# Optimization experiments

Hardware: AMD Instinct MI355X
Metric: run time of the kernel (lower is better)

The kernel has to match this reference:

```python
import jax, jax.numpy as jnp
import numpy as np

N = 50000   # total nodes across batch of graphs
E = 600000  # edges (avg degree 12)
D = 128     # feature dim
L = 3       # GNN layers
B = 64      # number of graphs


def setup_inputs() -> dict:
    key = jax.random.key(0)
    ks = jax.random.split(key, 9)
    x = jax.random.normal(ks[0], (N, D), dtype=jnp.float32)
    edge_index = jax.random.randint(ks[1], (2, E), 0, N)
    batch = jnp.sort(jax.random.randint(ks[2], (N,), 0, B))
    # hard one-hot architecture gates (output of ST gumbel-softmax)
    z_agg = jax.nn.one_hot(jax.random.randint(ks[3], (L,), 0, 3), 3, dtype=jnp.float32)
    z_pool = jax.nn.one_hot(jax.random.randint(ks[4], (), 0, 3), 3, dtype=jnp.float32)
    scale = 1.0 / np.sqrt(D)
    W1 = jax.random.normal(ks[5], (L, D, D), dtype=jnp.float32) * scale
    b1 = jnp.zeros((L, D), dtype=jnp.float32)
    W2 = jax.random.normal(ks[6], (L, D, D), dtype=jnp.float32) * scale
    b2 = jnp.zeros((L, D), dtype=jnp.float32)
    return {"x": x, "edge_index": edge_index, "batch": batch,
            "z_agg": z_agg, "z_pool": z_pool,
            "W1": W1, "b1": b1, "W2": W2, "b2": b2}


def reference(x, edge_index, batch, z_agg, z_pool, W1, b1, W2, b2):
    src, dst = edge_index[0], edge_index[1]
    ones_e = jnp.ones((E,), dtype=x.dtype)
    deg = jax.ops.segment_sum(ones_e, dst, num_segments=N)          # [N]
    deg_c = jnp.maximum(deg, 1.0)[:, None]
    has_nb = (deg > 0)[:, None]

    for l in range(L):
        msg = x[src]                                                # [E, D] gather
        s = jax.ops.segment_sum(msg, dst, num_segments=N)           # sum aggr
        m = s / deg_c                                               # mean aggr
        mx = jax.ops.segment_max(msg, dst, num_segments=N)          # max aggr
        mx = jnp.where(has_nb, mx, 0.0)                             # PyG fills empty with 0
        agg = z_agg[l, 0] * s + z_agg[l, 1] * m + z_agg[l, 2] * mx
        # combine='sum' then FeedForwardNetwork: Linear->relu->Linear
        h = x + agg
        h = jnp.maximum(h @ W1[l] + b1[l], 0.0)
        h = h @ W2[l] + b2[l]
        # act='relu', layer_connect='skip_sum'
        x = x + jnp.maximum(h, 0.0)

    # global pooling mixture over batch vector
    ps = jax.ops.segment_sum(x, batch, num_segments=B)              # [B, D]
    cnt = jax.ops.segment_sum(jnp.ones((N,), x.dtype), batch, num_segments=B)
    pm = ps / jnp.maximum(cnt, 1.0)[:, None]
    pmx = jax.ops.segment_max(x, batch, num_segments=B)
    pmx = jnp.where((cnt > 0)[:, None], pmx, 0.0)
    return z_pool[0] * ps + z_pool[1] * pm + z_pool[2] * pmx
```

## Files before the change

kernel.cpp:

```cpp
#include <hip/hip_runtime.h>
#include <cfloat>

#define DD 128
#define NLAYERS 3
#define NPB 128
#define SCHUNK 1024

typedef short bf16x8 __attribute__((ext_vector_type(8)));
typedef float f32x4 __attribute__((ext_vector_type(4)));

__device__ __forceinline__ unsigned short f2b(float f) {
    unsigned u = __float_as_uint(f);
    u += 0x7fffu + ((u >> 16) & 1u);
    return (unsigned short)(u >> 16);
}
__device__ __forceinline__ float b2f(unsigned short b) {
    return __uint_as_float(((unsigned)b) << 16);
}

__device__ __forceinline__ unsigned enc_f(float f) {
    unsigned b = __float_as_uint(f);
    return (b & 0x80000000u) ? ~b : (b | 0x80000000u);
}
__device__ __forceinline__ float dec_f(unsigned u) {
    return __uint_as_float((u & 0x80000000u) ? (u & 0x7fffffffu) : ~u);
}

__global__ void convert_xb_kernel(const float* __restrict__ in,
                                  unsigned short* __restrict__ xb,
                                  int* __restrict__ deg,
                                  float* __restrict__ ps, unsigned* __restrict__ pmx,
                                  int* __restrict__ cnt,
                                  int n4, int nN, int nBD, int nB) {
    int i = blockIdx.x * blockDim.x + threadIdx.x;
    if (i < n4) {
        float4 v = ((const float4*)in)[i];
        ushort4 b;
        b.x = f2b(v.x); b.y = f2b(v.y); b.z = f2b(v.z); b.w = f2b(v.w);
        ((ushort4*)xb)[i] = b;
    }
    if (i < nN) deg[i] = 0;
    if (i < nBD) { ps[i] = 0.f; pmx[i] = 0u; }
    if (i < nB) cnt[i] = 0;
}

__global__ void convert_w_kernel(const float* __restrict__ W1s, const float* __restrict__ W2s,
                                 unsigned short* __restrict__ Wb1s,
                                 unsigned short* __restrict__ Wb2s, int per) {
    int idx = blockIdx.x * blockDim.x + threadIdx.x;
    if (idx >= 2 * per) return;
    const float* W = (idx < per) ? W1s : W2s;
    unsigned short* Wb = (idx < per) ? Wb1s : Wb2s;
    if (idx >= per) idx -= per;
    int lane = idx & 63;
    int rest = idx >> 6;
    int ks = rest & 3; rest >>= 2;
    int nt = rest & 7;
    int l  = rest >> 3;
    int n = nt * 16 + (lane & 15);
    int kbase = ks * 32 + (lane >> 4) * 8;
    const float* Wl = W + (size_t)l * DD * DD;
    unsigned short* dst = Wb + (size_t)l * DD * DD + ((size_t)(nt * 4 + ks) * 64 + lane) * 8;
#pragma unroll
    for (int j = 0; j < 8; ++j) dst[j] = f2b(Wl[(size_t)(kbase + j) * DD + n]);
}


__global__ void deg_kernel(const int* __restrict__ dst, int* __restrict__ deg, int nE) {
    int e = blockIdx.x * blockDim.x + threadIdx.x;
    if (e < nE) atomicAdd(&deg[dst[e]], 1);
}

__global__ __launch_bounds__(256) void scan_sum_kernel(const int* __restrict__ deg,
                                                       int* __restrict__ bsum, int nN) {
    int t = threadIdx.x;
    int base = blockIdx.x * SCHUNK + t * 4;
    int v = 0;
#pragma unroll
    for (int k = 0; k < 4; ++k) { int i = base + k; if (i < nN) v += deg[i]; }
    for (int off = 32; off; off >>= 1) v += __shfl_down(v, off, 64);
    __shared__ int wsum[4];
    if ((t & 63) == 0) wsum[t >> 6] = v;
    __syncthreads();
    if (t == 0) bsum[blockIdx.x] = wsum[0] + wsum[1] + wsum[2] + wsum[3];
}

__global__ __launch_bounds__(256) void scan_top_kernel(const int* __restrict__ bsum,
                                                       int* __restrict__ boff,
                                                       int* __restrict__ row_ptr,
                                                       int G, int nN) {
    __shared__ int sh[256];
    int t = threadIdx.x;
    int v = (t < G) ? bsum[t] : 0;
    sh[t] = v;
    __syncthreads();
    for (int off = 1; off < 256; off <<= 1) {
        int o = (t >= off) ? sh[t - off] : 0;
        __syncthreads();
        sh[t] += o;
        __syncthreads();
    }
    if (t < G) boff[t] = sh[t] - v;
    if (t == 255) row_ptr[nN] = sh[255];
}

__global__ __launch_bounds__(256) void scan_apply_kernel(const int* __restrict__ deg,
                                                         const int* __restrict__ boff,
                                                         int* __restrict__ row_ptr, int nN) {
    __shared__ int sh[256];
    int t = threadIdx.x;
    int base = blockIdx.x * SCHUNK + t * 4;
    int d0 = 0, d1 = 0, d2 = 0, d3 = 0;
    if (base + 0 < nN) d0 = deg[base + 0];
    if (base + 1 < nN) d1 = deg[base + 1];
    if (base + 2 < nN) d2 = deg[base + 2];
    if (base + 3 < nN) d3 = deg[base + 3];
    int tsum = d0 + d1 + d2 + d3;
    sh[t] = tsum;
    __syncthreads();
    for (int off = 1; off < 256; off <<= 1) {
        int o = (t >= off) ? sh[t - off] : 0;
        __syncthreads();
        sh[t] += o;
        __syncthreads();
    }
    int run = boff[blockIdx.x] + sh[t] - tsum;
    if (base + 0 < nN) row_ptr[base + 0] = run;           run += d0;
    if (base + 1 < nN) row_ptr[base + 1] = run;           run += d1;
    if (base + 2 < nN) row_ptr[base + 2] = run;           run += d2;
    if (base + 3 < nN) row_ptr[base + 3] = run;
}

__global__ void fill_kernel(const int* __restrict__ src, const int* __restrict__ dst,
                            const int* __restrict__ row_ptr, int* __restrict__ deg,
                            int* __restrict__ csr_src, int nE) {
    int e = blockIdx.x * blockDim.x + threadIdx.x;
    if (e >= nE) return;
    int d = dst[e];
    int pos = row_ptr[d] + atomicSub(&deg[d], 1) - 1;
    csr_src[pos] = src[e];
}

__global__ __launch_bounds__(256) void agg_combine_kernel(const unsigned short* __restrict__ xb,
                                                          const int* __restrict__ csr_src,
                                                          const int* __restrict__ row_ptr,
                                                          const float* __restrict__ z_agg_l,
                                                          unsigned short* __restrict__ h0b,
                                                          int nN) {
    int t = threadIdx.x;
    int n = blockIdx.x * 8 + (t >> 5);
    if (n >= nN) return;
    int q = t & 31;
    int start = row_ptr[n], end = row_ptr[n + 1];
    float za0 = z_agg_l[0], za1 = z_agg_l[1], za2 = z_agg_l[2];

    const ushort4* tab = (const ushort4*)xb;
    float4 sum = make_float4(0.f, 0.f, 0.f, 0.f);
    float4 mx  = make_float4(-FLT_MAX, -FLT_MAX, -FLT_MAX, -FLT_MAX);
    int last = end - 1;
    for (int e = start; e < end; e += 8) {
        int s0 = csr_src[e];
        int s1 = csr_src[e + 1 <= last ? e + 1 : last];
        int s2 = csr_src[e + 2 <= last ? e + 2 : last];
        int s3 = csr_src[e + 3 <= last ? e + 3 : last];
        int s4 = csr_src[e + 4 <= last ? e + 4 : last];
        int s5 = csr_src[e + 5 <= last ? e + 5 : last];
        int s6 = csr_src[e + 6 <= last ? e + 6 : last];
        int s7 = csr_src[e + 7 <= last ? e + 7 : last];
        ushort4 v0 = tab[(size_t)s0 * 32 + q];
        ushort4 v1 = tab[(size_t)s1 * 32 + q];
        ushort4 v2 = tab[(size_t)s2 * 32 + q];
        ushort4 v3 = tab[(size_t)s3 * 32 + q];
        ushort4 v4 = tab[(size_t)s4 * 32 + q];
        ushort4 v5 = tab[(size_t)s5 * 32 + q];
        ushort4 v6 = tab[(size_t)s6 * 32 + q];
        ushort4 v7 = tab[(size_t)s7 * 32 + q];
#define ACCP(vb, ok) { float ax=b2f(vb.x),ay=b2f(vb.y),az=b2f(vb.z),aw=b2f(vb.w); \
                  mx.x=fmaxf(mx.x,ax);mx.y=fmaxf(mx.y,ay); \
                  mx.z=fmaxf(mx.z,az);mx.w=fmaxf(mx.w,aw); \
                  if (ok) { sum.x+=ax;sum.y+=ay;sum.z+=az;sum.w+=aw; } }
        ACCP(v0, true)
        ACCP(v1, e + 1 < end)
        ACCP(v2, e + 2 < end)
        ACCP(v3, e + 3 < end)
        ACCP(v4, e + 4 < end)
        ACCP(v5, e + 5 < end)
        ACCP(v6, e + 6 < end)
        ACCP(v7, e + 7 < end)
#undef ACCP
    }
    int degn = end - start;
    float inv = 1.0f / fmaxf((float)degn, 1.0f);
    float c01 = za0 + za1 * inv;
    bool nb = (degn > 0);
    ushort4 sb = tab[(size_t)n * 32 + q];
    ushort4 r;
    r.x = f2b(b2f(sb.x) + c01 * sum.x + za2 * (nb ? mx.x : 0.f));
    r.y = f2b(b2f(sb.y) + c01 * sum.y + za2 * (nb ? mx.y : 0.f));
    r.z = f2b(b2f(sb.z) + c01 * sum.z + za2 * (nb ? mx.z : 0.f));
    r.w = f2b(b2f(sb.w) + c01 * sum.w + za2 * (nb ? mx.w : 0.f));
    ((ushort4*)(h0b + (size_t)n * DD))[q] = r;
}

__global__ __launch_bounds__(256) void fused_ffn_kernel(
        const unsigned short* __restrict__ h0b,
        const unsigned short* __restrict__ Wb1, const float* __restrict__ b1,
        const unsigned short* __restrict__ Wb2, const float* __restrict__ b2,
        const unsigned short* __restrict__ xb_in,
        unsigned short* __restrict__ xb_out, int M) {
    __shared__ char lds[64 * DD * 4];

    int t = threadIdx.x;
    int lane = t & 63;
    int w = t >> 6;
    int row0 = blockIdx.x * 64;
    int ar = row0 + w * 16 + (lane & 15);
    if (ar > M - 1) ar = M - 1;
    int g = lane >> 4;
    int colw = lane & 15;
    int rbl = w * 16 + g * 4;

    const unsigned short* Ap = h0b + (size_t)ar * DD + g * 8;
    bf16x8 a0 = *(const bf16x8*)(Ap);
    bf16x8 a1 = *(const bf16x8*)(Ap + 32);
    bf16x8 a2 = *(const bf16x8*)(Ap + 64);
    bf16x8 a3 = *(const bf16x8*)(Ap + 96);

    const bf16x8* Wv1 = (const bf16x8*)Wb1;
#pragma unroll
    for (int nt = 0; nt < 8; ++nt) {
        f32x4 acc = {0.f, 0.f, 0.f, 0.f};
        acc = __builtin_amdgcn_mfma_f32_16x16x32_bf16(a0, Wv1[(nt * 4 + 0) * 64 + lane], acc, 0, 0, 0);
        acc = __builtin_amdgcn_mfma_f32_16x16x32_bf16(a1, Wv1[(nt * 4 + 1) * 64 + lane], acc, 0, 0, 0);
        acc = __builtin_amdgcn_mfma_f32_16x16x32_bf16(a2, Wv1[(nt * 4 + 2) * 64 + lane], acc, 0, 0, 0);
        acc = __builtin_amdgcn_mfma_f32_16x16x32_bf16(a3, Wv1[(nt * 4 + 3) * 64 + lane], acc, 0, 0, 0);
        float bv = b1[nt * 16 + colw];
        int cb = (nt * 16 + colw) * 2;
#pragma unroll
        for (int i = 0; i < 4; ++i) {
            int r1 = rbl + i;
            *(unsigned short*)(lds + r1 * 256 + (cb ^ ((unsigned)(r1 & 7) << 4))) =
                f2b(fmaxf(acc[i] + bv, 0.f));
        }
    }

    int rAl = w * 16 + (lane & 15);
    unsigned swA = (unsigned)(rAl & 7) << 4;
    const char* hA = lds + rAl * 256;
    bf16x8 c0 = *(const bf16x8*)(hA + ((g * 16 +   0) ^ swA));
    bf16x8 c1 = *(const bf16x8*)(hA + ((g * 16 +  64) ^ swA));
    bf16x8 c2 = *(const bf16x8*)(hA + ((g * 16 + 128) ^ swA));
    bf16x8 c3 = *(const bf16x8*)(hA + ((g * 16 + 192) ^ swA));
    __syncthreads();

    const bf16x8* Wv2 = (const bf16x8*)Wb2;
#pragma unroll
    for (int nt = 0; nt < 8; ++nt) {
        f32x4 acc = {0.f, 0.f, 0.f, 0.f};
        acc = __builtin_amdgcn_mfma_f32_16x16x32_bf16(c0, Wv2[(nt * 4 + 0) * 64 + lane], acc, 0, 0, 0);
        acc = __builtin_amdgcn_mfma_f32_16x16x32_bf16(c1, Wv2[(nt * 4 + 1) * 64 + lane], acc, 0, 0, 0);
        acc = __builtin_amdgcn_mfma_f32_16x16x32_bf16(c2, Wv2[(nt * 4 + 2) * 64 + lane], acc, 0, 0, 0);
        acc = __builtin_amdgcn_mfma_f32_16x16x32_bf16(c3, Wv2[(nt * 4 + 3) * 64 + lane], acc, 0, 0, 0);
        float bv = b2[nt * 16 + colw];
        int cb = (nt * 16 + colw) * 4;
#pragma unroll
        for (int i = 0; i < 4; ++i) {
            int r1 = rbl + i;
            *(float*)(lds + r1 * 512 + (cb ^ ((unsigned)(r1 & 7) << 4))) =
                fmaxf(acc[i] + bv, 0.f);
        }
    }
    __syncthreads();

    int q = t & 31;
    int grp = t >> 5;
    for (int pass = 0; pass < 8; ++pass) {
        int rr = pass * 8 + grp;
        int n = row0 + rr;
        if (n < M) {
            ushort4 xv = ((const ushort4*)(xb_in + (size_t)n * DD))[q];
            float4 vv = *(const float4*)(lds + rr * 512 + ((q * 16) ^ ((unsigned)(rr & 7) << 4)));
            ushort4 b;
            b.x = f2b(b2f(xv.x) + vv.x);
            b.y = f2b(b2f(xv.y) + vv.y);
            b.z = f2b(b2f(xv.z) + vv.z);
            b.w = f2b(b2f(xv.w) + vv.w);
            ((ushort4*)(xb_out + (size_t)n * DD))[q] = b;
        }
    }
}

__global__ __launch_bounds__(256) void pool_partial_kernel(const unsigned short* __restrict__ xb,
                                                           const int* __restrict__ batch,
                                                           float* __restrict__ ps,
                                                           unsigned* __restrict__ pmx,
                                                           int* __restrict__ cnt, int nN) {
    int t = threadIdx.x;
    int q = t & 31;
    int p = t >> 5;
    int node0 = blockIdx.x * NPB;
    int nodeEnd = node0 + NPB; if (nodeEnd > nN) nodeEnd = nN;

    const ushort4* xv = (const ushort4*)xb;
    float4 sum = make_float4(0.f, 0.f, 0.f, 0.f);
    float4 mx  = make_float4(-FLT_MAX, -FLT_MAX, -FLT_MAX, -FLT_MAX);
    int count = 0, g_cur = -1;

    for (int row = node0 + p; row < nodeEnd; row += 8) {
        int g = batch[row];
        if (g != g_cur) {
            if (g_cur >= 0) {
                atomicAdd(&ps[(size_t)g_cur * DD + q * 4 + 0], sum.x);
                atomicAdd(&ps[(size_t)g_cur * DD + q * 4 + 1], sum.y);
                atomicAdd(&ps[(size_t)g_cur * DD + q * 4 + 2], sum.z);
                atomicAdd(&ps[(size_t)g_cur * DD + q * 4 + 3], sum.w);
                atomicMax(&pmx[(size_t)g_cur * DD + q * 4 + 0], enc_f(mx.x));
                atomicMax(&pmx[(size_t)g_cur * DD + q * 4 + 1], enc_f(mx.y));
                atomicMax(&pmx[(size_t)g_cur * DD + q * 4 + 2], enc_f(mx.z));
                atomicMax(&pmx[(size_t)g_cur * DD + q * 4 + 3], enc_f(mx.w));
                if (q == 0) atomicAdd(&cnt[g_cur], count);
            }
            sum = make_float4(0.f, 0.f, 0.f, 0.f);
            mx  = make_float4(-FLT_MAX, -FLT_MAX, -FLT_MAX, -FLT_MAX);
            count = 0; g_cur = g;
        }
        ushort4 vb = xv[(size_t)row * 32 + q];
        float vx = b2f(vb.x), vy = b2f(vb.y), vz = b2f(vb.z), vw = b2f(vb.w);
        sum.x += vx; sum.y += vy; sum.z += vz; sum.w += vw;
        mx.x = fmaxf(mx.x, vx); mx.y = fmaxf(mx.y, vy);
        mx.z = fmaxf(mx.z, vz); mx.w = fmaxf(mx.w, vw);
        count++;
    }
    if (g_cur >= 0) {
        atomicAdd(&ps[(size_t)g_cur * DD + q * 4 + 0], sum.x);
        atomicAdd(&ps[(size_t)g_cur * DD + q * 4 + 1], sum.y);
        atomicAdd(&ps[(size_t)g_cur * DD + q * 4 + 2], sum.z);
        atomicAdd(&ps[(size_t)g_cur * DD + q * 4 + 3], sum.w);
        atomicMax(&pmx[(size_t)g_cur * DD + q * 4 + 0], enc_f(mx.x));
        atomicMax(&pmx[(size_t)g_cur * DD + q * 4 + 1], enc_f(mx.y));
        atomicMax(&pmx[(size_t)g_cur * DD + q * 4 + 2], enc_f(mx.z));
        atomicMax(&pmx[(size_t)g_cur * DD + q * 4 + 3], enc_f(mx.w));
        if (q == 0) atomicAdd(&cnt[g_cur], count);
    }
}

__global__ void pool_final_kernel(const float* __restrict__ ps,
                                  const unsigned* __restrict__ pmx,
                                  const int* __restrict__ cnt,
                                  const float* __restrict__ z_pool,
                                  float* __restrict__ out, int total) {
    int i = blockIdx.x * blockDim.x + threadIdx.x;
    if (i >= total) return;
    int g = i >> 7;
    float zp0 = z_pool[0], zp1 = z_pool[1], zp2 = z_pool[2];
    int c = cnt[g];
    float s = ps[i];
    float pm = s / fmaxf((float)c, 1.0f);
    float pv = (c > 0) ? dec_f(pmx[i]) : 0.0f;
    out[i] = zp0 * s + zp1 * pm + zp2 * pv;
}

extern "C" void kernel_launch(void* const* d_in, const int* in_sizes, int n_in,
                              void* d_out, int out_size, void* d_ws, size_t ws_size,
                              hipStream_t stream) {
    const float* x_in   = (const float*)d_in[0];
    const int*   eidx   = (const int*)d_in[1];
    const int*   batch  = (const int*)d_in[2];
    const float* z_agg  = (const float*)d_in[3];
    const float* z_pool = (const float*)d_in[4];
    const float* W1     = (const float*)d_in[5];
    const float* b1     = (const float*)d_in[6];
    const float* W2     = (const float*)d_in[7];
    const float* b2     = (const float*)d_in[8];

    int nN = in_sizes[0] / DD;
    int nE = in_sizes[1] / 2;
    int nB = out_size / DD;
    const int* src = eidx;
    const int* dst = eidx + nE;

    char* p = (char*)d_ws;
    size_t nd = (size_t)nN * DD * sizeof(float);
    unsigned short* xb0 = (unsigned short*)p;  p += nd / 2;
    unsigned short* xbA = (unsigned short*)p;  p += nd / 2;
    unsigned short* h0b = (unsigned short*)p;  p += nd / 2;
    unsigned short* Wb1 = (unsigned short*)p;  p += (size_t)NLAYERS * DD * DD * 2;
    unsigned short* Wb2 = (unsigned short*)p;  p += (size_t)NLAYERS * DD * DD * 2;
    int* row_ptr = (int*)p;  p += (size_t)(nN + 1) * 4;
    int* deg     = (int*)p;  p += (size_t)nN * 4;
    int* csr_src = (int*)p;  p += (size_t)nE * 4;
    float*    ps  = (float*)p;    p += (size_t)nB * DD * 4;
    unsigned* pmx = (unsigned*)p; p += (size_t)nB * DD * 4;
    int*      cnt = (int*)p;      p += (size_t)nB * 4;
    int*      bsum = (int*)p;     p += 256 * 4;
    int*      boff = (int*)p;

    int G = (nN + SCHUNK - 1) / SCHUNK;

    int n4 = nN * DD / 4;
    convert_xb_kernel<<<(n4 + 255) / 256, 256, 0, stream>>>(x_in, xb0, deg, ps, pmx, cnt,
                                                            n4, nN, nB * DD, nB);
    int per = NLAYERS * 8 * 4 * 64;
    convert_w_kernel<<<(2 * per + 255) / 256, 256, 0, stream>>>(W1, W2, Wb1, Wb2, per);

    deg_kernel<<<(nE + 255) / 256, 256, 0, stream>>>(dst, deg, nE);
    scan_sum_kernel<<<G, 256, 0, stream>>>(deg, bsum, nN);
    scan_top_kernel<<<1, 256, 0, stream>>>(bsum, boff, row_ptr, G, nN);
    scan_apply_kernel<<<G, 256, 0, stream>>>(deg, boff, row_ptr, nN);
    fill_kernel<<<(nE + 255) / 256, 256, 0, stream>>>(src, dst, row_ptr, deg, csr_src, nE);

    int agrid = (nN + 7) / 8;
    int fgrid = (nN + 63) / 64;
    agg_combine_kernel<<<agrid, 256, 0, stream>>>(xb0, csr_src, row_ptr, z_agg + 0, h0b, nN);
    fused_ffn_kernel<<<fgrid, 256, 0, stream>>>(h0b, Wb1 + 0 * DD * DD, b1 + 0 * DD,
                                                Wb2 + 0 * DD * DD, b2 + 0 * DD,
                                                xb0, xbA, nN);
    agg_combine_kernel<<<agrid, 256, 0, stream>>>(xbA, csr_src, row_ptr, z_agg + 3, h0b, nN);
    fused_ffn_kernel<<<fgrid, 256, 0, stream>>>(h0b, Wb1 + 1 * DD * DD, b1 + 1 * DD,
                                                Wb2 + 1 * DD * DD, b2 + 1 * DD,
                                                xbA, xb0, nN);
    agg_combine_kernel<<<agrid, 256, 0, stream>>>(xb0, csr_src, row_ptr, z_agg + 6, h0b, nN);
    fused_ffn_kernel<<<fgrid, 256, 0, stream>>>(h0b, Wb1 + 2 * DD * DD, b1 + 2 * DD,
                                                Wb2 + 2 * DD * DD, b2 + 2 * DD,
                                                xb0, xbA, nN);

    pool_partial_kernel<<<(nN + NPB - 1) / NPB, 256, 0, stream>>>(xbA, batch, ps, pmx, cnt, nN);
    pool_final_kernel<<<(nB * DD + 255) / 256, 256, 0, stream>>>(ps, pmx, cnt, z_pool,
                                                                 (float*)d_out, nB * DD);
}
```

Measured before the change: 235.3 us.

## Merge init kernels, fold scan top into apply, widen gather to 16B loads

Combines the x and weight conversion launches into one kernel and folds the single-block top-level scan into each scan_apply block, so two kernel launches go away. The aggregation kernel now handles 16 nodes per block with 16 lanes each loading 8 bf16 values (16-byte loads), and unrolls the edge loop by 6 instead of 8. It also clamps source indices and pads csr_src. Every scan_apply block redundantly rescans bsum, and the per-thread register use in the gather changes.

```diff
diff --git a/kernel.cpp b/kernel.cpp
--- a/kernel.cpp
+++ b/kernel.cpp
@@ -8,6 +8,7 @@
 
 typedef short bf16x8 __attribute__((ext_vector_type(8)));
 typedef float f32x4 __attribute__((ext_vector_type(4)));
+typedef unsigned short u16x8 __attribute__((ext_vector_type(8)));
 
 __device__ __forceinline__ unsigned short f2b(float f) {
     unsigned u = __float_as_uint(f);
@@ -26,43 +27,44 @@
     return __uint_as_float((u & 0x80000000u) ? (u & 0x7fffffffu) : ~u);
 }
 
-__global__ void convert_xb_kernel(const float* __restrict__ in,
-                                  unsigned short* __restrict__ xb,
-                                  int* __restrict__ deg,
-                                  float* __restrict__ ps, unsigned* __restrict__ pmx,
-                                  int* __restrict__ cnt,
-                                  int n4, int nN, int nBD, int nB) {
-    int i = blockIdx.x * blockDim.x + threadIdx.x;
-    if (i < n4) {
-        float4 v = ((const float4*)in)[i];
-        ushort4 b;
-        b.x = f2b(v.x); b.y = f2b(v.y); b.z = f2b(v.z); b.w = f2b(v.w);
-        ((ushort4*)xb)[i] = b;
-    }
-    if (i < nN) deg[i] = 0;
-    if (i < nBD) { ps[i] = 0.f; pmx[i] = 0u; }
-    if (i < nB) cnt[i] = 0;
-}
-
-__global__ void convert_w_kernel(const float* __restrict__ W1s, const float* __restrict__ W2s,
-                                 unsigned short* __restrict__ Wb1s,
-                                 unsigned short* __restrict__ Wb2s, int per) {
-    int idx = blockIdx.x * blockDim.x + threadIdx.x;
-    if (idx >= 2 * per) return;
-    const float* W = (idx < per) ? W1s : W2s;
-    unsigned short* Wb = (idx < per) ? Wb1s : Wb2s;
-    if (idx >= per) idx -= per;
-    int lane = idx & 63;
-    int rest = idx >> 6;
-    int ks = rest & 3; rest >>= 2;
-    int nt = rest & 7;
-    int l  = rest >> 3;
-    int n = nt * 16 + (lane & 15);
-    int kbase = ks * 32 + (lane >> 4) * 8;
-    const float* Wl = W + (size_t)l * DD * DD;
-    unsigned short* dst = Wb + (size_t)l * DD * DD + ((size_t)(nt * 4 + ks) * 64 + lane) * 8;
-#pragma unroll
-    for (int j = 0; j < 8; ++j) dst[j] = f2b(Wl[(size_t)(kbase + j) * DD + n]);
+__global__ void convert_init_kernel(const float* __restrict__ x_in,
+                                    unsigned short* __restrict__ xb,
+                                    const float* __restrict__ W1s, const float* __restrict__ W2s,
+                                    unsigned short* __restrict__ Wb1s,
+                                    unsigned short* __restrict__ Wb2s,
+                                    int* __restrict__ deg,
+                                    float* __restrict__ ps, unsigned* __restrict__ pmx,
+                                    int* __restrict__ cnt,
+                                    int n4, int nN, int nBD, int nB, int per, int xbBlocks) {
+    if ((int)blockIdx.x < xbBlocks) {
+        int i = blockIdx.x * 256 + threadIdx.x;
+        if (i < n4) {
+            float4 v = ((const float4*)x_in)[i];
+            ushort4 b;
+            b.x = f2b(v.x); b.y = f2b(v.y); b.z = f2b(v.z); b.w = f2b(v.w);
+            ((ushort4*)xb)[i] = b;
+        }
+        if (i < nN) deg[i] = 0;
+        if (i < nBD) { ps[i] = 0.f; pmx[i] = 0u; }
+        if (i < nB) cnt[i] = 0;
+    } else {
+        int idx = (blockIdx.x - xbBlocks) * 256 + threadIdx.x;
+        if (idx >= 2 * per) return;
+        const float* W = (idx < per) ? W1s : W2s;
+        unsigned short* Wb = (idx < per) ? Wb1s : Wb2s;
+        if (idx >= per) idx -= per;
+        int lane = idx & 63;
+        int rest = idx >> 6;
+        int ks = rest & 3; rest >>= 2;
+        int nt = rest & 7;
+        int l  = rest >> 3;
+        int n = nt * 16 + (lane & 15);
+        int kbase = ks * 32 + (lane >> 4) * 8;
+        const float* Wl = W + (size_t)l * DD * DD;
+        unsigned short* dst = Wb + (size_t)l * DD * DD + ((size_t)(nt * 4 + ks) * 64 + lane) * 8;
+#pragma unroll
+        for (int j = 0; j < 8; ++j) dst[j] = f2b(Wl[(size_t)(kbase + j) * DD + n]);
+    }
 }
 
 
@@ -85,29 +87,12 @@
     if (t == 0) bsum[blockIdx.x] = wsum[0] + wsum[1] + wsum[2] + wsum[3];
 }
 
-__global__ __launch_bounds__(256) void scan_top_kernel(const int* __restrict__ bsum,
-                                                       int* __restrict__ boff,
-                                                       int* __restrict__ row_ptr,
-                                                       int G, int nN) {
+__global__ __launch_bounds__(256) void scan_apply_kernel(const int* __restrict__ deg,
+                                                         const int* __restrict__ bsum,
+                                                         int* __restrict__ row_ptr,
+                                                         int nN, int G) {
     __shared__ int sh[256];
-    int t = threadIdx.x;
-    int v = (t < G) ? bsum[t] : 0;
-    sh[t] = v;
-    __syncthreads();
-    for (int off = 1; off < 256; off <<= 1) {
-        int o = (t >= off) ? sh[t - off] : 0;
-        __syncthreads();
-        sh[t] += o;
-        __syncthreads();
-    }
-    if (t < G) boff[t] = sh[t] - v;
-    if (t == 255) row_ptr[nN] = sh[255];
-}
-
-__global__ __launch_bounds__(256) void scan_apply_kernel(const int* __restrict__ deg,
-                                                         const int* __restrict__ boff,
-                                                         int* __restrict__ row_ptr, int nN) {
-    __shared__ int sh[256];
+    __shared__ int sh2[256];
     int t = threadIdx.x;
     int base = blockIdx.x * SCHUNK + t * 4;
     int d0 = 0, d1 = 0, d2 = 0, d3 = 0;
@@ -117,18 +102,22 @@
     if (base + 3 < nN) d3 = deg[base + 3];
     int tsum = d0 + d1 + d2 + d3;
     sh[t] = tsum;
+    sh2[t] = (t < G) ? bsum[t] : 0;
     __syncthreads();
     for (int off = 1; off < 256; off <<= 1) {
-        int o = (t >= off) ? sh[t - off] : 0;
+        int o  = (t >= off) ? sh[t - off]  : 0;
+        int o2 = (t >= off) ? sh2[t - off] : 0;
         __syncthreads();
-        sh[t] += o;
+        sh[t] += o; sh2[t] += o2;
         __syncthreads();
     }
-    int run = boff[blockIdx.x] + sh[t] - tsum;
+    int bb = (blockIdx.x > 0) ? sh2[blockIdx.x - 1] : 0;
+    int run = bb + sh[t] - tsum;
     if (base + 0 < nN) row_ptr[base + 0] = run;           run += d0;
     if (base + 1 < nN) row_ptr[base + 1] = run;           run += d1;
     if (base + 2 < nN) row_ptr[base + 2] = run;           run += d2;
     if (base + 3 < nN) row_ptr[base + 3] = run;
+    if (blockIdx.x == G - 1 && t == 0) row_ptr[nN] = sh2[G - 1];
 }
 
 __global__ void fill_kernel(const int* __restrict__ src, const int* __restrict__ dst,
@@ -148,58 +137,60 @@
                                                           unsigned short* __restrict__ h0b,
                                                           int nN) {
     int t = threadIdx.x;
-    int n = blockIdx.x * 8 + (t >> 5);
+    int n = blockIdx.x * 16 + (t >> 4);
     if (n >= nN) return;
-    int q = t & 31;
+    int q = t & 15;
     int start = row_ptr[n], end = row_ptr[n + 1];
     float za0 = z_agg_l[0], za1 = z_agg_l[1], za2 = z_agg_l[2];
 
-    const ushort4* tab = (const ushort4*)xb;
-    float4 sum = make_float4(0.f, 0.f, 0.f, 0.f);
-    float4 mx  = make_float4(-FLT_MAX, -FLT_MAX, -FLT_MAX, -FLT_MAX);
+    const u16x8* tab = (const u16x8*)xb;
+    float sum[8], mx[8];
+#pragma unroll
+    for (int j = 0; j < 8; ++j) { sum[j] = 0.f; mx[j] = -FLT_MAX; }
+
     int last = end - 1;
-    for (int e = start; e < end; e += 8) {
-        int s0 = csr_src[e];
-        int s1 = csr_src[e + 1 <= last ? e + 1 : last];
-        int s2 = csr_src[e + 2 <= last ? e + 2 : last];
-        int s3 = csr_src[e + 3 <= last ? e + 3 : last];
-        int s4 = csr_src[e + 4 <= last ? e + 4 : last];
-        int s5 = csr_src[e + 5 <= last ? e + 5 : last];
-        int s6 = csr_src[e + 6 <= last ? e + 6 : last];
-        int s7 = csr_src[e + 7 <= last ? e + 7 : last];
-        ushort4 v0 = tab[(size_t)s0 * 32 + q];
-        ushort4 v1 = tab[(size_t)s1 * 32 + q];
-        ushort4 v2 = tab[(size_t)s2 * 32 + q];
-        ushort4 v3 = tab[(size_t)s3 * 32 + q];
-        ushort4 v4 = tab[(size_t)s4 * 32 + q];
-        ushort4 v5 = tab[(size_t)s5 * 32 + q];
-        ushort4 v6 = tab[(size_t)s6 * 32 + q];
-        ushort4 v7 = tab[(size_t)s7 * 32 + q];
-#define ACCP(vb, ok) { float ax=b2f(vb.x),ay=b2f(vb.y),az=b2f(vb.z),aw=b2f(vb.w); \
-                  mx.x=fmaxf(mx.x,ax);mx.y=fmaxf(mx.y,ay); \
-                  mx.z=fmaxf(mx.z,az);mx.w=fmaxf(mx.w,aw); \
-                  if (ok) { sum.x+=ax;sum.y+=ay;sum.z+=az;sum.w+=aw; } }
+    for (int e = start; e < end; e += 6) {
+        int idx[6];
+#pragma unroll
+        for (int k = 0; k < 6; ++k) {
+            int ee = e + k; ee = ee <= last ? ee : last;
+            int s = csr_src[ee];
+            s = s < 0 ? 0 : (s >= nN ? nN - 1 : s);
+            idx[k] = s;
+        }
+        u16x8 v0 = tab[(size_t)idx[0] * 16 + q];
+        u16x8 v1 = tab[(size_t)idx[1] * 16 + q];
+        u16x8 v2 = tab[(size_t)idx[2] * 16 + q];
+        u16x8 v3 = tab[(size_t)idx[3] * 16 + q];
+        u16x8 v4 = tab[(size_t)idx[4] * 16 + q];
+        u16x8 v5 = tab[(size_t)idx[5] * 16 + q];
+#define ACCP(vb, ok) { \
+        _Pragma("unroll") \
+        for (int j = 0; j < 8; ++j) { \
+            float f = b2f(vb[j]); \
+            mx[j] = fmaxf(mx[j], f); \
+            if (ok) sum[j] += f; \
+        } }
         ACCP(v0, true)
         ACCP(v1, e + 1 < end)
         ACCP(v2, e + 2 < end)
         ACCP(v3, e + 3 < end)
         ACCP(v4, e + 4 < end)
         ACCP(v5, e + 5 < end)
-        ACCP(v6, e + 6 < end)
-        ACCP(v7, e + 7 < end)
 #undef ACCP
     }
     int degn = end - start;
     float inv = 1.0f / fmaxf((float)degn, 1.0f);
     float c01 = za0 + za1 * inv;
     bool nb = (degn > 0);
-    ushort4 sb = tab[(size_t)n * 32 + q];
-    ushort4 r;
-    r.x = f2b(b2f(sb.x) + c01 * sum.x + za2 * (nb ? mx.x : 0.f));
-    r.y = f2b(b2f(sb.y) + c01 * sum.y + za2 * (nb ? mx.y : 0.f));
-    r.z = f2b(b2f(sb.z) + c01 * sum.z + za2 * (nb ? mx.z : 0.f));
-    r.w = f2b(b2f(sb.w) + c01 * sum.w + za2 * (nb ? mx.w : 0.f));
-    ((ushort4*)(h0b + (size_t)n * DD))[q] = r;
+    u16x8 sb = tab[(size_t)n * 16 + q];
+    u16x8 r;
+#pragma unroll
+    for (int j = 0; j < 8; ++j) {
+        float m = nb ? mx[j] : 0.f;
+        r[j] = f2b(b2f(sb[j]) + c01 * sum[j] + za2 * m);
+    }
+    ((u16x8*)h0b)[(size_t)n * 16 + q] = r;
 }
 
 __global__ __launch_bounds__(256) void fused_ffn_kernel(
@@ -388,28 +379,28 @@
     unsigned short* Wb2 = (unsigned short*)p;  p += (size_t)NLAYERS * DD * DD * 2;
     int* row_ptr = (int*)p;  p += (size_t)(nN + 1) * 4;
     int* deg     = (int*)p;  p += (size_t)nN * 4;
-    int* csr_src = (int*)p;  p += (size_t)nE * 4;
+    int* csr_src = (int*)p;  p += (size_t)nE * 4 + 64;
     float*    ps  = (float*)p;    p += (size_t)nB * DD * 4;
     unsigned* pmx = (unsigned*)p; p += (size_t)nB * DD * 4;
     int*      cnt = (int*)p;      p += (size_t)nB * 4;
-    int*      bsum = (int*)p;     p += 256 * 4;
-    int*      boff = (int*)p;
+    int*      bsum = (int*)p;
 
     int G = (nN + SCHUNK - 1) / SCHUNK;
 
     int n4 = nN * DD / 4;
-    convert_xb_kernel<<<(n4 + 255) / 256, 256, 0, stream>>>(x_in, xb0, deg, ps, pmx, cnt,
-                                                            n4, nN, nB * DD, nB);
     int per = NLAYERS * 8 * 4 * 64;
-    convert_w_kernel<<<(2 * per + 255) / 256, 256, 0, stream>>>(W1, W2, Wb1, Wb2, per);
+    int xbBlocks = (n4 + 255) / 256;
+    int wBlocks = (2 * per + 255) / 256;
+    convert_init_kernel<<<xbBlocks + wBlocks, 256, 0, stream>>>(
+        x_in, xb0, W1, W2, Wb1, Wb2, deg, ps, pmx, cnt,
+        n4, nN, nB * DD, nB, per, xbBlocks);
 
     deg_kernel<<<(nE + 255) / 256, 256, 0, stream>>>(dst, deg, nE);
     scan_sum_kernel<<<G, 256, 0, stream>>>(deg, bsum, nN);
-    scan_top_kernel<<<1, 256, 0, stream>>>(bsum, boff, row_ptr, G, nN);
-    scan_apply_kernel<<<G, 256, 0, stream>>>(deg, boff, row_ptr, nN);
+    scan_apply_kernel<<<G, 256, 0, stream>>>(deg, bsum, row_ptr, nN, G);
     fill_kernel<<<(nE + 255) / 256, 256, 0, stream>>>(src, dst, row_ptr, deg, csr_src, nE);
 
-    int agrid = (nN + 7) / 8;
+    int agrid = (nN + 15) / 16;
     int fgrid = (nN + 63) / 64;
     agg_combine_kernel<<<agrid, 256, 0, stream>>>(xb0, csr_src, row_ptr, z_agg + 0, h0b, nN);
     fused_ffn_kernel<<<fgrid, 256, 0, stream>>>(h0b, Wb1 + 0 * DD * DD, b1 + 0 * DD,
```

Result: slower. 267.7 us (+13.8%).
